# Kernel tuning notes

Measured on AMD Instinct MI355X. Metric: run time of the kernel, lower is better.

Reference implementation:

```python
import jax, jax.numpy as jnp
import numpy as np

B, N, DIM = 2, 2048, 1024
HEADS, DIM_HEAD, ROT = 16, 64, 32
SCALE = DIM_HEAD ** -0.5
INNER = HEADS * DIM_HEAD


def rotate_half(x):
    # '... (j d) -> ... j d' with j=2 -> split into first/second half
    d = x.shape[-1] // 2
    x1, x2 = x[..., :d], x[..., d:]
    return jnp.concatenate([-x2, x1], axis=-1)


def apply_rotary_pos_emb(freqs, t):
    rot = freqs.shape[-1]
    t1, t_pass = t[..., :rot], t[..., rot:]
    t1 = t1 * jnp.cos(freqs) + rotate_half(t1) * jnp.sin(freqs)
    return jnp.concatenate([t1, t_pass], axis=-1)


def setup_inputs() -> dict:
    key = jax.random.key(0)
    ks = jax.random.split(key, 5)
    x = jax.random.normal(ks[0], (B, N, DIM), dtype=jnp.float32)
    mask = jnp.ones((B, N), dtype=bool)
    rotary_pos_emb = jax.random.normal(ks[1], (N, ROT), dtype=jnp.float32)
    w_qkv = jax.random.normal(ks[2], (DIM, 3 * INNER), dtype=jnp.float32) * (DIM ** -0.5)
    w_out = jax.random.normal(ks[3], (INNER, DIM), dtype=jnp.float32) * (INNER ** -0.5)
    g = jnp.ones((DIM,), dtype=jnp.float32)
    return {"x": x, "mask": mask, "rotary_pos_emb": rotary_pos_emb,
            "w_qkv": w_qkv, "w_out": w_out, "g": g}


def reference(x, mask, rotary_pos_emb, w_qkv, w_out, g):
    b, n, _ = x.shape
    qkv = x @ w_qkv  # [b, n, 3*inner]
    q, k, v = jnp.split(qkv, 3, axis=-1)
    def to_heads(t):
        return t.reshape(b, n, HEADS, DIM_HEAD).transpose(0, 2, 1, 3)  # b h n d
    q, k, v = to_heads(q), to_heads(k), to_heads(v)
    q = q * SCALE
    # note: original applies rotary to q, k AND v
    q = apply_rotary_pos_emb(rotary_pos_emb, q)
    k = apply_rotary_pos_emb(rotary_pos_emb, k)
    v = apply_rotary_pos_emb(rotary_pos_emb, v)
    sim = jnp.einsum('bhid,bhjd->bhij', q, k)  # [b, h, n, n]
    neg = -jnp.finfo(sim.dtype).max
    sim = jnp.where(mask[:, None, None, :], sim, neg)
    causal_mask = jnp.triu(jnp.ones((n, n), dtype=bool), 1)
    sim = jnp.where(causal_mask, neg, sim)
    attn = jax.nn.softmax(sim.astype(jnp.float32), axis=-1).astype(sim.dtype)
    out = jnp.einsum('bhij,bhjd->bhid', attn, v)
    out = out.transpose(0, 2, 1, 3).reshape(b, n, INNER)
    out = out @ w_out
    # LayerNorm (no bias), eps=1e-5 for fp32, biased variance
    mean = jnp.mean(out, axis=-1, keepdims=True)
    var = jnp.var(out, axis=-1, keepdims=True)
    return (out - mean) * jax.lax.rsqrt(var + 1e-5) * g
```

## Files before the change

kernel.cpp:

```cpp
#include <hip/hip_runtime.h>
#include <stdint.h>

typedef unsigned short u16;
typedef __bf16 bf16x8 __attribute__((ext_vector_type(8)));
typedef float f32x4 __attribute__((ext_vector_type(4)));

#define B_ 2
#define N_ 2048
#define H_ 16
#define SCALE_ 0.125f
#define FM_ 11.0f

__device__ __forceinline__ float b2f(u16 u) {
    unsigned v = (unsigned)u << 16;
    float f;
    __builtin_memcpy(&f, &v, 4);
    return f;
}
__device__ __forceinline__ u16 f2b(float f) {
    unsigned x;
    __builtin_memcpy(&x, &f, 4);
    x = x + 0x7fff + ((x >> 16) & 1);
    return (u16)(x >> 16);
}
__device__ __forceinline__ unsigned fbits(float f) {
    unsigned x;
    __builtin_memcpy(&x, &f, 4);
    return x;
}

typedef const __attribute__((address_space(1))) unsigned int ga_uint;
typedef __attribute__((address_space(3))) unsigned int ls_uint;
__device__ __forceinline__ void gld_lds16(const void* g, void* l) {
    __builtin_amdgcn_global_load_lds((ga_uint*)g, (ls_uint*)l, 16, 0, 0);
}

#define MFMA_ __builtin_amdgcn_mfma_f32_16x16x32_bf16
#define ZERO4_ ((f32x4){0.f, 0.f, 0.f, 0.f})

__global__ __launch_bounds__(256) void sentinel(float* __restrict__ out, int n, float val) {
    int i = blockIdx.x * 256 + threadIdx.x;
    if (i < n) out[i] = val;
}

__global__ __launch_bounds__(256) void prep(const float* __restrict__ rotf,
                                            float* __restrict__ ct, float* __restrict__ st,
                                            const float* __restrict__ x, u16* __restrict__ xbf,
                                            const float* __restrict__ wqkv, u16* __restrict__ wqkvT,
                                            const float* __restrict__ wout, u16* __restrict__ woutT) {
    __shared__ float tile[32][33];
    int bid = blockIdx.x;
    const int tid = threadIdx.x;
    if (bid < 256) {
        int i = bid * 256 + tid;
        float f = rotf[i];
        ct[i] = cosf(f);
        st[i] = sinf(f);
        return;
    }
    bid -= 256;
    if (bid < 4096) {
        int i = (bid * 256 + tid) * 4;
        float4 v = *(const float4*)(x + i);
        ushort4 o;
        o.x = f2b(v.x); o.y = f2b(v.y); o.z = f2b(v.z); o.w = f2b(v.w);
        *(ushort4*)(xbf + i) = o;
        return;
    }
    bid -= 4096;
    const float* in;
    u16* out;
    int C, bx, by;
    if (bid < 3072) {
        in = wqkv; out = wqkvT; C = 3072; bx = bid % 96; by = bid / 96;
    } else {
        bid -= 3072;
        in = wout; out = woutT; C = 1024; bx = bid % 32; by = bid / 32;
    }
    const int R = 1024;
    int tx = tid & 31, ty = tid >> 5;
    int c0 = bx * 32, r0 = by * 32;
#pragma unroll
    for (int i = 0; i < 32; i += 8) tile[ty + i][tx] = in[(size_t)(r0 + ty + i) * C + c0 + tx];
    __syncthreads();
#pragma unroll
    for (int i = 0; i < 32; i += 8) out[(size_t)(c0 + ty + i) * R + r0 + tx] = f2b(tile[tx][ty + i]);
}

__global__ __launch_bounds__(256) void gemm_qkv(const u16* __restrict__ A, const u16* __restrict__ Bt,
                                                const float* __restrict__ ct, const float* __restrict__ st,
                                                u16* __restrict__ qo, u16* __restrict__ ko,
                                                u16* __restrict__ vt) {
    __shared__ __align__(16) u16 As[128 * 32];
    __shared__ __align__(16) u16 Bs[128 * 32];
    const int tid = threadIdx.x;
    const int wave = tid >> 6, lane = tid & 63;
    const int l15 = lane & 15, q4 = lane >> 4;
    const int id = blockIdx.x;
    const int xcd = id & 7, slot = id >> 3;
    const int nt = (xcd & 1) * 12 + (slot % 12);
    const int mt = (xcd >> 1) * 8 + (slot / 12);
    const int m0 = mt * 128, n0 = nt * 128;
    const int wm = (wave & 1) * 64, wn = (wave >> 1) * 64;
    const int lrow = lane >> 2, lchunk = (lane & 3) * 8;
    f32x4 c00 = ZERO4_, c01 = ZERO4_, c02 = ZERO4_, c03 = ZERO4_;
    f32x4 c10 = ZERO4_, c11 = ZERO4_, c12 = ZERO4_, c13 = ZERO4_;
    f32x4 c20 = ZERO4_, c21 = ZERO4_, c22 = ZERO4_, c23 = ZERO4_;
    f32x4 c30 = ZERO4_, c31 = ZERO4_, c32 = ZERO4_, c33 = ZERO4_;

    for (int k0 = 0; k0 < 1024; k0 += 32) {
        {
            int r0_ = wave * 32, r1_ = r0_ + 16;
            gld_lds16(&A[(size_t)(m0 + r0_ + lrow) * 1024 + k0 + lchunk], &As[r0_ * 32]);
            gld_lds16(&Bt[(size_t)(n0 + r0_ + lrow) * 1024 + k0 + lchunk], &Bs[r0_ * 32]);
            gld_lds16(&A[(size_t)(m0 + r1_ + lrow) * 1024 + k0 + lchunk], &As[r1_ * 32]);
            gld_lds16(&Bt[(size_t)(n0 + r1_ + lrow) * 1024 + k0 + lchunk], &Bs[r1_ * 32]);
        }
        __syncthreads();
        bf16x8 a0 = *(const bf16x8*)&As[(wm + l15) * 32 + q4 * 8];
        bf16x8 a1 = *(const bf16x8*)&As[(wm + 16 + l15) * 32 + q4 * 8];
        bf16x8 a2 = *(const bf16x8*)&As[(wm + 32 + l15) * 32 + q4 * 8];
        bf16x8 a3 = *(const bf16x8*)&As[(wm + 48 + l15) * 32 + q4 * 8];
        bf16x8 b0 = *(const bf16x8*)&Bs[(wn + l15) * 32 + q4 * 8];
        bf16x8 b1 = *(const bf16x8*)&Bs[(wn + 16 + l15) * 32 + q4 * 8];
        bf16x8 b2 = *(const bf16x8*)&Bs[(wn + 32 + l15) * 32 + q4 * 8];
        bf16x8 b3 = *(const bf16x8*)&Bs[(wn + 48 + l15) * 32 + q4 * 8];
        c00 = MFMA_(a0, b0, c00, 0, 0, 0); c01 = MFMA_(a0, b1, c01, 0, 0, 0);
        c02 = MFMA_(a0, b2, c02, 0, 0, 0); c03 = MFMA_(a0, b3, c03, 0, 0, 0);
        c10 = MFMA_(a1, b0, c10, 0, 0, 0); c11 = MFMA_(a1, b1, c11, 0, 0, 0);
        c12 = MFMA_(a1, b2, c12, 0, 0, 0); c13 = MFMA_(a1, b3, c13, 0, 0, 0);
        c20 = MFMA_(a2, b0, c20, 0, 0, 0); c21 = MFMA_(a2, b1, c21, 0, 0, 0);
        c22 = MFMA_(a2, b2, c22, 0, 0, 0); c23 = MFMA_(a2, b3, c23, 0, 0, 0);
        c30 = MFMA_(a3, b0, c30, 0, 0, 0); c31 = MFMA_(a3, b1, c31, 0, 0, 0);
        c32 = MFMA_(a3, b2, c32, 0, 0, 0); c33 = MFMA_(a3, b3, c33, 0, 0, 0);
        __syncthreads();
    }
    const int qh = n0 + wn;
    const int t = qh >> 10;
    const int h = (qh & 1023) >> 6;
    auto epi = [&](int mtb, f32x4 x0v, f32x4 x1v, f32x4 x2v, f32x4 x3v) {
#pragma unroll
        for (int r = 0; r < 4; r++) {
            int gm = m0 + wm + mtb + q4 * 4 + r;
            int b = gm >> 11, n = gm & 2047;
            float x0 = x0v[r], x1 = x1v[r], x2 = x2v[r], x3 = x3v[r];
            float c1 = ct[n * 32 + l15], s1 = st[n * 32 + l15];
            float c2 = ct[n * 32 + 16 + l15], s2 = st[n * 32 + 16 + l15];
            if (t == 0) { x0 *= SCALE_; x1 *= SCALE_; x2 *= SCALE_; x3 *= SCALE_; }
            float r0 = x0 * c1 - x1 * s1;
            float r1 = x1 * c2 + x0 * s2;
            int bh = b * H_ + h;
            if (t == 2) {
                u16* o = vt + (size_t)bh * 64 * N_;
                o[(l15) * N_ + n] = f2b(r0);
                o[(l15 + 16) * N_ + n] = f2b(r1);
                o[(l15 + 32) * N_ + n] = f2b(x2);
                o[(l15 + 48) * N_ + n] = f2b(x3);
            } else {
                u16* dst = (t == 0) ? qo : ko;
                u16* p = dst + ((size_t)bh * N_ + n) * 64;
                p[l15] = f2b(r0);
                p[l15 + 16] = f2b(r1);
                p[l15 + 32] = f2b(x2);
                p[l15 + 48] = f2b(x3);
            }
        }
    };
    epi(0, c00, c01, c02, c03);
    epi(16, c10, c11, c12, c13);
    epi(32, c20, c21, c22, c23);
    epi(48, c30, c31, c32, c33);
}

__global__ __launch_bounds__(256) void attn(const u16* __restrict__ q, const u16* __restrict__ k,
                                            const u16* __restrict__ vt, u16* __restrict__ out) {
    __shared__ __align__(16) u16 Ks[2][64 * 72];
    __shared__ __align__(16) u16 Vs[2][64 * 72];
    __shared__ __align__(16) u16 Ps[64 * 72];
    const int tid = threadIdx.x, wave = tid >> 6, lane = tid & 63;
    const int l15 = lane & 15, q4 = lane >> 4;
    const int id = blockIdx.x;
    const int slot = id >> 3;
    const int bh = (id & 7) * 4 + (slot >> 4);
    const int ta = slot & 15, tb = 31 - ta;
    const u16* qp = q + (size_t)bh * N_ * 64;
    const u16* kp = k + (size_t)bh * N_ * 64;
    const u16* vp = vt + (size_t)bh * 64 * N_;
    const int b = bh >> 4, h = bh & 15;
    const int srow8 = tid >> 3, scol8 = (tid & 7) * 8;
    const int prow = (wave * 16 + l15) * 72;

    bf16x8 aqA0, aqA1, aqB0, aqB1;
    {
        int qr = ta * 64 + wave * 16;
        aqA0 = *(const bf16x8*)&qp[(qr + l15) * 64 + q4 * 8];
        aqA1 = *(const bf16x8*)&qp[(qr + l15) * 64 + 32 + q4 * 8];
        qr = tb * 64 + wave * 16;
        aqB0 = *(const bf16x8*)&qp[(qr + l15) * 64 + q4 * 8];
        aqB1 = *(const bf16x8*)&qp[(qr + l15) * 64 + 32 + q4 * 8];
    }
    f32x4 o[4];
#pragma unroll
    for (int i = 0; i < 4; i++) o[i] = ZERO4_;
    float psum = 0.f;

    auto stage = [&](int jt, int buf) {
#pragma unroll
        for (int i = 0; i < 64; i += 32) {
            *(uint4*)&Ks[buf][(i + srow8) * 72 + scol8] =
                *(const uint4*)&kp[(size_t)(jt * 64 + i + srow8) * 64 + scol8];
            *(uint4*)&Vs[buf][(i + srow8) * 72 + scol8] =
                *(const uint4*)&vp[(size_t)(i + srow8) * N_ + jt * 64 + scol8];
        }
    };
    auto iter = [&](bf16x8 aq0, bf16x8 aq1, int cur, int domask, int qa, int jb) {
#pragma unroll
        for (int kt = 0; kt < 4; kt++) {
            bf16x8 kf0 = *(const bf16x8*)&Ks[cur][(kt * 16 + l15) * 72 + q4 * 8];
            bf16x8 kf1 = *(const bf16x8*)&Ks[cur][(kt * 16 + l15) * 72 + 32 + q4 * 8];
            f32x4 z = ZERO4_;
            z = MFMA_(kf0, aq0, z, 0, 0, 0);
            z = MFMA_(kf1, aq1, z, 0, 0, 0);
            float p0, p1, p2, p3;
            {
                float s0 = z[0], s1 = z[1], s2 = z[2], s3 = z[3];
                if (domask) {
                    int key = jb * 64 + kt * 16 + q4 * 4;
                    if (key + 0 > qa) s0 = -1e30f;
                    if (key + 1 > qa) s1 = -1e30f;
                    if (key + 2 > qa) s2 = -1e30f;
                    if (key + 3 > qa) s3 = -1e30f;
                }
                p0 = __expf(s0 - FM_); p1 = __expf(s1 - FM_);
                p2 = __expf(s2 - FM_); p3 = __expf(s3 - FM_);
            }
            psum += (p0 + p1) + (p2 + p3);
            uint2 pk;
            pk.x = __builtin_amdgcn_perm(fbits(p1), fbits(p0), 0x07060302u);
            pk.y = __builtin_amdgcn_perm(fbits(p3), fbits(p2), 0x07060302u);
            *(uint2*)&Ps[prow + kt * 16 + q4 * 4] = pk;
        }
        bf16x8 pf0 = *(const bf16x8*)&Ps[prow + q4 * 8];
        bf16x8 pf1 = *(const bf16x8*)&Ps[prow + 32 + q4 * 8];
#pragma unroll
        for (int dt = 0; dt < 4; dt++) {
            bf16x8 v0 = *(const bf16x8*)&Vs[cur][(dt * 16 + l15) * 72 + q4 * 8];
            bf16x8 v1 = *(const bf16x8*)&Vs[cur][(dt * 16 + l15) * 72 + 32 + q4 * 8];
            o[dt] = MFMA_(v0, pf0, o[dt], 0, 0, 0);
            o[dt] = MFMA_(v1, pf1, o[dt], 0, 0, 0);
        }
    };
    auto epilogue = [&](int qt) {
        float v = psum;
        v += __shfl_xor(v, 16);
        v += __shfl_xor(v, 32);
        float inv = 1.f / v;
        int n = qt * 64 + wave * 16 + l15;
        u16* op = out + ((size_t)b * N_ + n) * 1024 + h * 64;
#pragma unroll
        for (int dt = 0; dt < 4; dt++) {
            union { u16 u[4]; uint2 v2; } w;
#pragma unroll
            for (int r = 0; r < 4; r++) w.u[r] = f2b(o[dt][r] * inv);
            *(uint2*)(op + dt * 16 + q4 * 4) = w.v2;
        }
#pragma unroll
        for (int i = 0; i < 4; i++) o[i] = ZERO4_;
        psum = 0.f;
    };

    stage(0, 0);
    int m = 0;
    for (int jb = 0; jb <= ta; jb++, m++) {
        int cur = m & 1;
        __syncthreads();
        stage((jb < ta) ? (jb + 1) : 0, cur ^ 1);
        iter(aqA0, aqA1, cur, jb == ta, ta * 64 + wave * 16 + l15, jb);
    }
    epilogue(ta);
    for (int jb = 0; jb <= tb; jb++, m++) {
        int cur = m & 1;
        __syncthreads();
        if (jb < tb) stage(jb + 1, cur ^ 1);
        iter(aqB0, aqB1, cur, jb == tb, tb * 64 + wave * 16 + l15, jb);
    }
    epilogue(tb);
}

__global__ __launch_bounds__(256) void gemm_out(const u16* __restrict__ A, const u16* __restrict__ Bt,
                                                float* __restrict__ C) {
    __shared__ __align__(16) u16 As[128 * 32];
    __shared__ __align__(16) u16 Bs[128 * 32];
    const int tid = threadIdx.x;
    const int wave = tid >> 6, lane = tid & 63;
    const int l15 = lane & 15, q4 = lane >> 4;
    const int id = blockIdx.x;
    const int xcd = id & 7, slot = id >> 3;
    const int mt = xcd * 4 + (slot >> 3);
    const int nt = slot & 7;
    const int m0 = mt * 128, n0 = nt * 128;
    const int wm = (wave & 1) * 64, wn = (wave >> 1) * 64;
    const int lrow = lane >> 2, lchunk = (lane & 3) * 8;
    f32x4 c00 = ZERO4_, c01 = ZERO4_, c02 = ZERO4_, c03 = ZERO4_;
    f32x4 c10 = ZERO4_, c11 = ZERO4_, c12 = ZERO4_, c13 = ZERO4_;
    f32x4 c20 = ZERO4_, c21 = ZERO4_, c22 = ZERO4_, c23 = ZERO4_;
    f32x4 c30 = ZERO4_, c31 = ZERO4_, c32 = ZERO4_, c33 = ZERO4_;

    for (int k0 = 0; k0 < 1024; k0 += 32) {
        {
            int r0_ = wave * 32, r1_ = r0_ + 16;
            gld_lds16(&A[(size_t)(m0 + r0_ + lrow) * 1024 + k0 + lchunk], &As[r0_ * 32]);
            gld_lds16(&Bt[(size_t)(n0 + r0_ + lrow) * 1024 + k0 + lchunk], &Bs[r0_ * 32]);
            gld_lds16(&A[(size_t)(m0 + r1_ + lrow) * 1024 + k0 + lchunk], &As[r1_ * 32]);
            gld_lds16(&Bt[(size_t)(n0 + r1_ + lrow) * 1024 + k0 + lchunk], &Bs[r1_ * 32]);
        }
        __syncthreads();
        bf16x8 a0 = *(const bf16x8*)&As[(wm + l15) * 32 + q4 * 8];
        bf16x8 a1 = *(const bf16x8*)&As[(wm + 16 + l15) * 32 + q4 * 8];
        bf16x8 a2 = *(const bf16x8*)&As[(wm + 32 + l15) * 32 + q4 * 8];
        bf16x8 a3 = *(const bf16x8*)&As[(wm + 48 + l15) * 32 + q4 * 8];
        bf16x8 b0 = *(const bf16x8*)&Bs[(wn + l15) * 32 + q4 * 8];
        bf16x8 b1 = *(const bf16x8*)&Bs[(wn + 16 + l15) * 32 + q4 * 8];
        bf16x8 b2 = *(const bf16x8*)&Bs[(wn + 32 + l15) * 32 + q4 * 8];
        bf16x8 b3 = *(const bf16x8*)&Bs[(wn + 48 + l15) * 32 + q4 * 8];
        c00 = MFMA_(a0, b0, c00, 0, 0, 0); c01 = MFMA_(a0, b1, c01, 0, 0, 0);
        c02 = MFMA_(a0, b2, c02, 0, 0, 0); c03 = MFMA_(a0, b3, c03, 0, 0, 0);
        c10 = MFMA_(a1, b0, c10, 0, 0, 0); c11 = MFMA_(a1, b1, c11, 0, 0, 0);
        c12 = MFMA_(a1, b2, c12, 0, 0, 0); c13 = MFMA_(a1, b3, c13, 0, 0, 0);
        c20 = MFMA_(a2, b0, c20, 0, 0, 0); c21 = MFMA_(a2, b1, c21, 0, 0, 0);
        c22 = MFMA_(a2, b2, c22, 0, 0, 0); c23 = MFMA_(a2, b3, c23, 0, 0, 0);
        c30 = MFMA_(a3, b0, c30, 0, 0, 0); c31 = MFMA_(a3, b1, c31, 0, 0, 0);
        c32 = MFMA_(a3, b2, c32, 0, 0, 0); c33 = MFMA_(a3, b3, c33, 0, 0, 0);
        __syncthreads();
    }
    auto sto = [&](int mtb, int ntb, f32x4 c) {
#pragma unroll
        for (int r = 0; r < 4; r++) {
            int gm = m0 + wm + mtb + q4 * 4 + r;
            int gn = n0 + wn + ntb + l15;
            C[(size_t)gm * 1024 + gn] = c[r];
        }
    };
    sto(0, 0, c00);  sto(0, 16, c01);  sto(0, 32, c02);  sto(0, 48, c03);
    sto(16, 0, c10); sto(16, 16, c11); sto(16, 32, c12); sto(16, 48, c13);
    sto(32, 0, c20); sto(32, 16, c21); sto(32, 32, c22); sto(32, 48, c23);
    sto(48, 0, c30); sto(48, 16, c31); sto(48, 32, c32); sto(48, 48, c33);
}

__global__ __launch_bounds__(256) void lnorm(const float* __restrict__ x, const float* __restrict__ g,
                                             float* __restrict__ out) {
    __shared__ float sh[8];
    int row = blockIdx.x, tid = threadIdx.x;
    float4 v = *(const float4*)(x + (size_t)row * 1024 + tid * 4);
    float s = v.x + v.y + v.z + v.w;
    float sq = v.x * v.x + v.y * v.y + v.z * v.z + v.w * v.w;
#pragma unroll
    for (int m = 1; m < 64; m <<= 1) {
        s += __shfl_xor(s, m);
        sq += __shfl_xor(sq, m);
    }
    if ((tid & 63) == 0) {
        sh[tid >> 6] = s;
        sh[4 + (tid >> 6)] = sq;
    }
    __syncthreads();
    s = sh[0] + sh[1] + sh[2] + sh[3];
    sq = sh[4] + sh[5] + sh[6] + sh[7];
    float mean = s * (1.f / 1024.f);
    float var = fmaxf(sq * (1.f / 1024.f) - mean * mean, 0.f);
    float rstd = rsqrtf(var + 1e-5f);
    float4 gv = *(const float4*)(g + tid * 4);
    float4 ov;
    ov.x = (v.x - mean) * rstd * gv.x;
    ov.y = (v.y - mean) * rstd * gv.y;
    ov.z = (v.z - mean) * rstd * gv.z;
    ov.w = (v.w - mean) * rstd * gv.w;
    *(float4*)(out + (size_t)row * 1024 + tid * 4) = ov;
}

extern "C" void kernel_launch(void* const* d_in, const int* in_sizes, int n_in,
                              void* d_out, int out_size, void* d_ws, size_t ws_size,
                              hipStream_t stream) {
    const float* x = nullptr;
    const float* rotf = nullptr;
    const float* wqkv = nullptr;
    const float* wout = nullptr;
    const float* g = nullptr;
    for (int i = 0; i < n_in; i++) {
        switch (in_sizes[i]) {
            case 4194304: x = (const float*)d_in[i]; break;
            case 65536:   rotf = (const float*)d_in[i]; break;
            case 3145728: wqkv = (const float*)d_in[i]; break;
            case 1048576: wout = (const float*)d_in[i]; break;
            case 1024:    g = (const float*)d_in[i]; break;
            default: break;
        }
    }
    int oblk = (out_size + 255) / 256;
    if (!(x && rotf && wqkv && wout && g)) {
        sentinel<<<oblk, 256, 0, stream>>>((float*)d_out, out_size, 200.f);
        return;
    }
    const size_t MB = 1024u * 1024;
    if (ws_size < 80 * MB) {
        sentinel<<<oblk, 256, 0, stream>>>((float*)d_out, out_size, 100.f);
        return;
    }
    char* ws = (char*)d_ws;
    u16* wqkvT = (u16*)(ws);
    u16* woutT = (u16*)(ws + 6 * MB);
    u16* xbf = (u16*)(ws + 8 * MB);
    u16* qbuf = (u16*)(ws + 16 * MB);
    u16* kbuf = (u16*)(ws + 24 * MB);
    u16* vtbuf = (u16*)(ws + 32 * MB);
    u16* abuf = (u16*)(ws + 40 * MB);
    float* pbuf = (float*)(ws + 48 * MB);
    float* ctab = (float*)(ws + 64 * MB);
    float* stab = (float*)(ws + 64 * MB + 256 * 1024);

    prep<<<8448, 256, 0, stream>>>(rotf, ctab, stab, x, xbf, wqkv, wqkvT, wout, woutT);
    gemm_qkv<<<768, 256, 0, stream>>>(xbf, wqkvT, ctab, stab, qbuf, kbuf, vtbuf);
    attn<<<512, 256, 0, stream>>>(qbuf, kbuf, vtbuf, abuf);
    gemm_out<<<256, 256, 0, stream>>>(abuf, woutT, pbuf);
    lnorm<<<4096, 256, 0, stream>>>(pbuf, g, (float*)d_out);
}
```

Before: 203.5 us.

## Double-buffer and swizzle LDS tiles in QKV and output GEMMs

Both projection GEMMs switch from a single LDS tile with two syncthreads per k-step to a two-stage double buffer. The next tile's global-to-LDS loads are issued before the MFMAs, with explicit vmcnt/lgkmcnt waits, raw s_barrier and sched_barrier fences. The LDS layout is XOR-swizzled by row, with the inverse mapping applied to the global source addresses, to cut bank conflicts on the 16-byte fragment reads. s_setprio raises wave priority around the MFMA block; the cost is double the LDS footprint and more hand-ordered synchronization.

```diff
diff --git a/kernel.cpp b/kernel.cpp
--- a/kernel.cpp
+++ b/kernel.cpp
@@ -87,12 +87,21 @@
     for (int i = 0; i < 32; i += 8) out[(size_t)(c0 + ty + i) * R + r0 + tx] = f2b(tile[tx][ty + i]);
 }
 
+__device__ __forceinline__ int swz_off(int row, int c16) {
+    return (((row * 64 + c16 * 16) ^ ((row & 7) << 4)) >> 1);
+}
+__device__ __forceinline__ void swz_inv(int W, int& r, int& c16) {
+    int rh = W >> 7;
+    r = (rh << 1) | (((W >> 6) & 1) ^ ((rh >> 1) & 1));
+    c16 = ((W >> 4) & 3) ^ (r & 3);
+}
+
 __global__ __launch_bounds__(256) void gemm_qkv(const u16* __restrict__ A, const u16* __restrict__ Bt,
                                                 const float* __restrict__ ct, const float* __restrict__ st,
                                                 u16* __restrict__ qo, u16* __restrict__ ko,
                                                 u16* __restrict__ vt) {
-    __shared__ __align__(16) u16 As[128 * 32];
-    __shared__ __align__(16) u16 Bs[128 * 32];
+    __shared__ __align__(16) u16 As[2][128 * 32];
+    __shared__ __align__(16) u16 Bs[2][128 * 32];
     const int tid = threadIdx.x;
     const int wave = tid >> 6, lane = tid & 63;
     const int l15 = lane & 15, q4 = lane >> 4;
@@ -102,29 +111,55 @@
     const int mt = (xcd >> 1) * 8 + (slot / 12);
     const int m0 = mt * 128, n0 = nt * 128;
     const int wm = (wave & 1) * 64, wn = (wave >> 1) * 64;
-    const int lrow = lane >> 2, lchunk = (lane & 3) * 8;
+
+    int rS0, cS0, rS1, cS1;
+    swz_inv((wave * 32) * 64 + lane * 16, rS0, cS0);
+    swz_inv((wave * 32 + 16) * 64 + lane * 16, rS1, cS1);
+    const u16* aS0 = A + (size_t)(m0 + rS0) * 1024 + cS0 * 8;
+    const u16* aS1 = A + (size_t)(m0 + rS1) * 1024 + cS1 * 8;
+    const u16* bS0 = Bt + (size_t)(n0 + rS0) * 1024 + cS0 * 8;
+    const u16* bS1 = Bt + (size_t)(n0 + rS1) * 1024 + cS1 * 8;
+
+    auto stage = [&](int buf, int k0) {
+        gld_lds16(aS0 + k0, &As[buf][(wave * 32) * 32]);
+        gld_lds16(bS0 + k0, &Bs[buf][(wave * 32) * 32]);
+        gld_lds16(aS1 + k0, &As[buf][(wave * 32 + 16) * 32]);
+        gld_lds16(bS1 + k0, &Bs[buf][(wave * 32 + 16) * 32]);
+    };
+    const int oa0 = swz_off(wm + l15, q4), oa1 = swz_off(wm + 16 + l15, q4),
+              oa2 = swz_off(wm + 32 + l15, q4), oa3 = swz_off(wm + 48 + l15, q4);
+    const int ob0 = swz_off(wn + l15, q4), ob1 = swz_off(wn + 16 + l15, q4),
+              ob2 = swz_off(wn + 32 + l15, q4), ob3 = swz_off(wn + 48 + l15, q4);
+
     f32x4 c00 = ZERO4_, c01 = ZERO4_, c02 = ZERO4_, c03 = ZERO4_;
     f32x4 c10 = ZERO4_, c11 = ZERO4_, c12 = ZERO4_, c13 = ZERO4_;
     f32x4 c20 = ZERO4_, c21 = ZERO4_, c22 = ZERO4_, c23 = ZERO4_;
     f32x4 c30 = ZERO4_, c31 = ZERO4_, c32 = ZERO4_, c33 = ZERO4_;
 
-    for (int k0 = 0; k0 < 1024; k0 += 32) {
-        {
-            int r0_ = wave * 32, r1_ = r0_ + 16;
-            gld_lds16(&A[(size_t)(m0 + r0_ + lrow) * 1024 + k0 + lchunk], &As[r0_ * 32]);
-            gld_lds16(&Bt[(size_t)(n0 + r0_ + lrow) * 1024 + k0 + lchunk], &Bs[r0_ * 32]);
-            gld_lds16(&A[(size_t)(m0 + r1_ + lrow) * 1024 + k0 + lchunk], &As[r1_ * 32]);
-            gld_lds16(&Bt[(size_t)(n0 + r1_ + lrow) * 1024 + k0 + lchunk], &Bs[r1_ * 32]);
-        }
-        __syncthreads();
-        bf16x8 a0 = *(const bf16x8*)&As[(wm + l15) * 32 + q4 * 8];
-        bf16x8 a1 = *(const bf16x8*)&As[(wm + 16 + l15) * 32 + q4 * 8];
-        bf16x8 a2 = *(const bf16x8*)&As[(wm + 32 + l15) * 32 + q4 * 8];
-        bf16x8 a3 = *(const bf16x8*)&As[(wm + 48 + l15) * 32 + q4 * 8];
-        bf16x8 b0 = *(const bf16x8*)&Bs[(wn + l15) * 32 + q4 * 8];
-        bf16x8 b1 = *(const bf16x8*)&Bs[(wn + 16 + l15) * 32 + q4 * 8];
-        bf16x8 b2 = *(const bf16x8*)&Bs[(wn + 32 + l15) * 32 + q4 * 8];
-        bf16x8 b3 = *(const bf16x8*)&Bs[(wn + 48 + l15) * 32 + q4 * 8];
+    stage(0, 0);
+    stage(1, 32);
+    int kNext = 64;
+    for (int i = 0; i < 31; ++i) {
+        const int cur = i & 1;
+        asm volatile("s_waitcnt vmcnt(4)" ::: "memory");
+        __builtin_amdgcn_sched_barrier(0);
+        __builtin_amdgcn_s_barrier();
+        __builtin_amdgcn_sched_barrier(0);
+        bf16x8 a0 = *(const bf16x8*)&As[cur][oa0];
+        bf16x8 a1 = *(const bf16x8*)&As[cur][oa1];
+        bf16x8 a2 = *(const bf16x8*)&As[cur][oa2];
+        bf16x8 a3 = *(const bf16x8*)&As[cur][oa3];
+        bf16x8 b0 = *(const bf16x8*)&Bs[cur][ob0];
+        bf16x8 b1 = *(const bf16x8*)&Bs[cur][ob1];
+        bf16x8 b2 = *(const bf16x8*)&Bs[cur][ob2];
+        bf16x8 b3 = *(const bf16x8*)&Bs[cur][ob3];
+        asm volatile("s_waitcnt lgkmcnt(0)" ::: "memory");
+        __builtin_amdgcn_sched_barrier(0);
+        __builtin_amdgcn_s_barrier();
+        __builtin_amdgcn_sched_barrier(0);
+        if (i < 30) { stage(cur, kNext); kNext += 32; }
+        __builtin_amdgcn_sched_barrier(0);
+        __builtin_amdgcn_s_setprio(1);
         c00 = MFMA_(a0, b0, c00, 0, 0, 0); c01 = MFMA_(a0, b1, c01, 0, 0, 0);
         c02 = MFMA_(a0, b2, c02, 0, 0, 0); c03 = MFMA_(a0, b3, c03, 0, 0, 0);
         c10 = MFMA_(a1, b0, c10, 0, 0, 0); c11 = MFMA_(a1, b1, c11, 0, 0, 0);
@@ -133,7 +168,29 @@
         c22 = MFMA_(a2, b2, c22, 0, 0, 0); c23 = MFMA_(a2, b3, c23, 0, 0, 0);
         c30 = MFMA_(a3, b0, c30, 0, 0, 0); c31 = MFMA_(a3, b1, c31, 0, 0, 0);
         c32 = MFMA_(a3, b2, c32, 0, 0, 0); c33 = MFMA_(a3, b3, c33, 0, 0, 0);
-        __syncthreads();
+        __builtin_amdgcn_s_setprio(0);
+    }
+    {
+        asm volatile("s_waitcnt vmcnt(0)" ::: "memory");
+        __builtin_amdgcn_sched_barrier(0);
+        __builtin_amdgcn_s_barrier();
+        __builtin_amdgcn_sched_barrier(0);
+        bf16x8 a0 = *(const bf16x8*)&As[1][oa0];
+        bf16x8 a1 = *(const bf16x8*)&As[1][oa1];
+        bf16x8 a2 = *(const bf16x8*)&As[1][oa2];
+        bf16x8 a3 = *(const bf16x8*)&As[1][oa3];
+        bf16x8 b0 = *(const bf16x8*)&Bs[1][ob0];
+        bf16x8 b1 = *(const bf16x8*)&Bs[1][ob1];
+        bf16x8 b2 = *(const bf16x8*)&Bs[1][ob2];
+        bf16x8 b3 = *(const bf16x8*)&Bs[1][ob3];
+        c00 = MFMA_(a0, b0, c00, 0, 0, 0); c01 = MFMA_(a0, b1, c01, 0, 0, 0);
+        c02 = MFMA_(a0, b2, c02, 0, 0, 0); c03 = MFMA_(a0, b3, c03, 0, 0, 0);
+        c10 = MFMA_(a1, b0, c10, 0, 0, 0); c11 = MFMA_(a1, b1, c11, 0, 0, 0);
+        c12 = MFMA_(a1, b2, c12, 0, 0, 0); c13 = MFMA_(a1, b3, c13, 0, 0, 0);
+        c20 = MFMA_(a2, b0, c20, 0, 0, 0); c21 = MFMA_(a2, b1, c21, 0, 0, 0);
+        c22 = MFMA_(a2, b2, c22, 0, 0, 0); c23 = MFMA_(a2, b3, c23, 0, 0, 0);
+        c30 = MFMA_(a3, b0, c30, 0, 0, 0); c31 = MFMA_(a3, b1, c31, 0, 0, 0);
+        c32 = MFMA_(a3, b2, c32, 0, 0, 0); c33 = MFMA_(a3, b3, c33, 0, 0, 0);
     }
     const int qh = n0 + wn;
     const int t = qh >> 10;
@@ -289,8 +346,8 @@
 
 __global__ __launch_bounds__(256) void gemm_out(const u16* __restrict__ A, const u16* __restrict__ Bt,
                                                 float* __restrict__ C) {
-    __shared__ __align__(16) u16 As[128 * 32];
-    __shared__ __align__(16) u16 Bs[128 * 32];
+    __shared__ __align__(16) u16 As[2][128 * 32];
+    __shared__ __align__(16) u16 Bs[2][128 * 32];
     const int tid = threadIdx.x;
     const int wave = tid >> 6, lane = tid & 63;
     const int l15 = lane & 15, q4 = lane >> 4;
@@ -300,29 +357,55 @@
     const int nt = slot & 7;
     const int m0 = mt * 128, n0 = nt * 128;
     const int wm = (wave & 1) * 64, wn = (wave >> 1) * 64;
-    const int lrow = lane >> 2, lchunk = (lane & 3) * 8;
+
+    int rS0, cS0, rS1, cS1;
+    swz_inv((wave * 32) * 64 + lane * 16, rS0, cS0);
+    swz_inv((wave * 32 + 16) * 64 + lane * 16, rS1, cS1);
+    const u16* aS0 = A + (size_t)(m0 + rS0) * 1024 + cS0 * 8;
+    const u16* aS1 = A + (size_t)(m0 + rS1) * 1024 + cS1 * 8;
+    const u16* bS0 = Bt + (size_t)(n0 + rS0) * 1024 + cS0 * 8;
+    const u16* bS1 = Bt + (size_t)(n0 + rS1) * 1024 + cS1 * 8;
+
+    auto stage = [&](int buf, int k0) {
+        gld_lds16(aS0 + k0, &As[buf][(wave * 32) * 32]);
+        gld_lds16(bS0 + k0, &Bs[buf][(wave * 32) * 32]);
+        gld_lds16(aS1 + k0, &As[buf][(wave * 32 + 16) * 32]);
+        gld_lds16(bS1 + k0, &Bs[buf][(wave * 32 + 16) * 32]);
+    };
+    const int oa0 = swz_off(wm + l15, q4), oa1 = swz_off(wm + 16 + l15, q4),
+              oa2 = swz_off(wm + 32 + l15, q4), oa3 = swz_off(wm + 48 + l15, q4);
+    const int ob0 = swz_off(wn + l15, q4), ob1 = swz_off(wn + 16 + l15, q4),
+              ob2 = swz_off(wn + 32 + l15, q4), ob3 = swz_off(wn + 48 + l15, q4);
+
     f32x4 c00 = ZERO4_, c01 = ZERO4_, c02 = ZERO4_, c03 = ZERO4_;
     f32x4 c10 = ZERO4_, c11 = ZERO4_, c12 = ZERO4_, c13 = ZERO4_;
     f32x4 c20 = ZERO4_, c21 = ZERO4_, c22 = ZERO4_, c23 = ZERO4_;
     f32x4 c30 = ZERO4_, c31 = ZERO4_, c32 = ZERO4_, c33 = ZERO4_;
 
-    for (int k0 = 0; k0 < 1024; k0 += 32) {
-        {
-            int r0_ = wave * 32, r1_ = r0_ + 16;
-            gld_lds16(&A[(size_t)(m0 + r0_ + lrow) * 1024 + k0 + lchunk], &As[r0_ * 32]);
-            gld_lds16(&Bt[(size_t)(n0 + r0_ + lrow) * 1024 + k0 + lchunk], &Bs[r0_ * 32]);
-            gld_lds16(&A[(size_t)(m0 + r1_ + lrow) * 1024 + k0 + lchunk], &As[r1_ * 32]);
-            gld_lds16(&Bt[(size_t)(n0 + r1_ + lrow) * 1024 + k0 + lchunk], &Bs[r1_ * 32]);
-        }
-        __syncthreads();
-        bf16x8 a0 = *(const bf16x8*)&As[(wm + l15) * 32 + q4 * 8];
-        bf16x8 a1 = *(const bf16x8*)&As[(wm + 16 + l15) * 32 + q4 * 8];
-        bf16x8 a2 = *(const bf16x8*)&As[(wm + 32 + l15) * 32 + q4 * 8];
-        bf16x8 a3 = *(const bf16x8*)&As[(wm + 48 + l15) * 32 + q4 * 8];
-        bf16x8 b0 = *(const bf16x8*)&Bs[(wn + l15) * 32 + q4 * 8];
-        bf16x8 b1 = *(const bf16x8*)&Bs[(wn + 16 + l15) * 32 + q4 * 8];
-        bf16x8 b2 = *(const bf16x8*)&Bs[(wn + 32 + l15) * 32 + q4 * 8];
-        bf16x8 b3 = *(const bf16x8*)&Bs[(wn + 48 + l15) * 32 + q4 * 8];
+    stage(0, 0);
+    stage(1, 32);
+    int kNext = 64;
+    for (int i = 0; i < 31; ++i) {
+        const int cur = i & 1;
+        asm volatile("s_waitcnt vmcnt(4)" ::: "memory");
+        __builtin_amdgcn_sched_barrier(0);
+        __builtin_amdgcn_s_barrier();
+        __builtin_amdgcn_sched_barrier(0);
+        bf16x8 a0 = *(const bf16x8*)&As[cur][oa0];
+        bf16x8 a1 = *(const bf16x8*)&As[cur][oa1];
+        bf16x8 a2 = *(const bf16x8*)&As[cur][oa2];
+        bf16x8 a3 = *(const bf16x8*)&As[cur][oa3];
+        bf16x8 b0 = *(const bf16x8*)&Bs[cur][ob0];
+        bf16x8 b1 = *(const bf16x8*)&Bs[cur][ob1];
+        bf16x8 b2 = *(const bf16x8*)&Bs[cur][ob2];
+        bf16x8 b3 = *(const bf16x8*)&Bs[cur][ob3];
+        asm volatile("s_waitcnt lgkmcnt(0)" ::: "memory");
+        __builtin_amdgcn_sched_barrier(0);
+        __builtin_amdgcn_s_barrier();
+        __builtin_amdgcn_sched_barrier(0);
+        if (i < 30) { stage(cur, kNext); kNext += 32; }
+        __builtin_amdgcn_sched_barrier(0);
+        __builtin_amdgcn_s_setprio(1);
         c00 = MFMA_(a0, b0, c00, 0, 0, 0); c01 = MFMA_(a0, b1, c01, 0, 0, 0);
         c02 = MFMA_(a0, b2, c02, 0, 0, 0); c03 = MFMA_(a0, b3, c03, 0, 0, 0);
         c10 = MFMA_(a1, b0, c10, 0, 0, 0); c11 = MFMA_(a1, b1, c11, 0, 0, 0);
@@ -331,7 +414,29 @@
         c22 = MFMA_(a2, b2, c22, 0, 0, 0); c23 = MFMA_(a2, b3, c23, 0, 0, 0);
         c30 = MFMA_(a3, b0, c30, 0, 0, 0); c31 = MFMA_(a3, b1, c31, 0, 0, 0);
         c32 = MFMA_(a3, b2, c32, 0, 0, 0); c33 = MFMA_(a3, b3, c33, 0, 0, 0);
-        __syncthreads();
+        __builtin_amdgcn_s_setprio(0);
+    }
+    {
+        asm volatile("s_waitcnt vmcnt(0)" ::: "memory");
+        __builtin_amdgcn_sched_barrier(0);
+        __builtin_amdgcn_s_barrier();
+        __builtin_amdgcn_sched_barrier(0);
+        bf16x8 a0 = *(const bf16x8*)&As[1][oa0];
+        bf16x8 a1 = *(const bf16x8*)&As[1][oa1];
+        bf16x8 a2 = *(const bf16x8*)&As[1][oa2];
+        bf16x8 a3 = *(const bf16x8*)&As[1][oa3];
+        bf16x8 b0 = *(const bf16x8*)&Bs[1][ob0];
+        bf16x8 b1 = *(const bf16x8*)&Bs[1][ob1];
+        bf16x8 b2 = *(const bf16x8*)&Bs[1][ob2];
+        bf16x8 b3 = *(const bf16x8*)&Bs[1][ob3];
+        c00 = MFMA_(a0, b0, c00, 0, 0, 0); c01 = MFMA_(a0, b1, c01, 0, 0, 0);
+        c02 = MFMA_(a0, b2, c02, 0, 0, 0); c03 = MFMA_(a0, b3, c03, 0, 0, 0);
+        c10 = MFMA_(a1, b0, c10, 0, 0, 0); c11 = MFMA_(a1, b1, c11, 0, 0, 0);
+        c12 = MFMA_(a1, b2, c12, 0, 0, 0); c13 = MFMA_(a1, b3, c13, 0, 0, 0);
+        c20 = MFMA_(a2, b0, c20, 0, 0, 0); c21 = MFMA_(a2, b1, c21, 0, 0, 0);
+        c22 = MFMA_(a2, b2, c22, 0, 0, 0); c23 = MFMA_(a2, b3, c23, 0, 0, 0);
+        c30 = MFMA_(a3, b0, c30, 0, 0, 0); c31 = MFMA_(a3, b1, c31, 0, 0, 0);
+        c32 = MFMA_(a3, b2, c32, 0, 0, 0); c33 = MFMA_(a3, b3, c33, 0, 0, 0);
     }
     auto sto = [&](int mtb, int ntb, f32x4 c) {
 #pragma unroll
```

Measured after the change: 217.0 us. 6.7% more time.

## Double-buffer LDS in both GEMMs and prefetch K/V tiles into registers in attention

Applied to the files above, without the earlier changes.

Both projection GEMMs now use two LDS buffers, issuing the next k-slice's global-to-LDS loads before computing on the current one, which removes one barrier per iteration. The attention kernel splits staging into a register prefetch issued one tile ahead and an LDS write after compute, using a single barrier with an explicit lgkmcnt wait. This is meant to hide global load latency behind MFMA work. The cost is doubled LDS use in the GEMMs, extra VGPRs in attention, and subtle ordering hazards: the GEMM loop relies on async LDS loads completing before the barrier (no explicit vmcnt wait shown), and reads of the current buffer may race with writes to the other buffer across iterations.

```diff
diff --git a/kernel.cpp b/kernel.cpp
--- a/kernel.cpp
+++ b/kernel.cpp
@@ -91,8 +91,8 @@
                                                 const float* __restrict__ ct, const float* __restrict__ st,
                                                 u16* __restrict__ qo, u16* __restrict__ ko,
                                                 u16* __restrict__ vt) {
-    __shared__ __align__(16) u16 As[128 * 32];
-    __shared__ __align__(16) u16 Bs[128 * 32];
+    __shared__ __align__(16) u16 As[2][128 * 32];
+    __shared__ __align__(16) u16 Bs[2][128 * 32];
     const int tid = threadIdx.x;
     const int wave = tid >> 6, lane = tid & 63;
     const int l15 = lane & 15, q4 = lane >> 4;
@@ -103,28 +103,33 @@
     const int m0 = mt * 128, n0 = nt * 128;
     const int wm = (wave & 1) * 64, wn = (wave >> 1) * 64;
     const int lrow = lane >> 2, lchunk = (lane & 3) * 8;
+
+    auto stage = [&](int buf, int k0) {
+        int r0_ = wave * 32, r1_ = r0_ + 16;
+        gld_lds16(&A[(size_t)(m0 + r0_ + lrow) * 1024 + k0 + lchunk], &As[buf][r0_ * 32]);
+        gld_lds16(&Bt[(size_t)(n0 + r0_ + lrow) * 1024 + k0 + lchunk], &Bs[buf][r0_ * 32]);
+        gld_lds16(&A[(size_t)(m0 + r1_ + lrow) * 1024 + k0 + lchunk], &As[buf][r1_ * 32]);
+        gld_lds16(&Bt[(size_t)(n0 + r1_ + lrow) * 1024 + k0 + lchunk], &Bs[buf][r1_ * 32]);
+    };
+
     f32x4 c00 = ZERO4_, c01 = ZERO4_, c02 = ZERO4_, c03 = ZERO4_;
     f32x4 c10 = ZERO4_, c11 = ZERO4_, c12 = ZERO4_, c13 = ZERO4_;
     f32x4 c20 = ZERO4_, c21 = ZERO4_, c22 = ZERO4_, c23 = ZERO4_;
     f32x4 c30 = ZERO4_, c31 = ZERO4_, c32 = ZERO4_, c33 = ZERO4_;
 
-    for (int k0 = 0; k0 < 1024; k0 += 32) {
-        {
-            int r0_ = wave * 32, r1_ = r0_ + 16;
-            gld_lds16(&A[(size_t)(m0 + r0_ + lrow) * 1024 + k0 + lchunk], &As[r0_ * 32]);
-            gld_lds16(&Bt[(size_t)(n0 + r0_ + lrow) * 1024 + k0 + lchunk], &Bs[r0_ * 32]);
-            gld_lds16(&A[(size_t)(m0 + r1_ + lrow) * 1024 + k0 + lchunk], &As[r1_ * 32]);
-            gld_lds16(&Bt[(size_t)(n0 + r1_ + lrow) * 1024 + k0 + lchunk], &Bs[r1_ * 32]);
-        }
-        __syncthreads();
-        bf16x8 a0 = *(const bf16x8*)&As[(wm + l15) * 32 + q4 * 8];
-        bf16x8 a1 = *(const bf16x8*)&As[(wm + 16 + l15) * 32 + q4 * 8];
-        bf16x8 a2 = *(const bf16x8*)&As[(wm + 32 + l15) * 32 + q4 * 8];
-        bf16x8 a3 = *(const bf16x8*)&As[(wm + 48 + l15) * 32 + q4 * 8];
-        bf16x8 b0 = *(const bf16x8*)&Bs[(wn + l15) * 32 + q4 * 8];
-        bf16x8 b1 = *(const bf16x8*)&Bs[(wn + 16 + l15) * 32 + q4 * 8];
-        bf16x8 b2 = *(const bf16x8*)&Bs[(wn + 32 + l15) * 32 + q4 * 8];
-        bf16x8 b3 = *(const bf16x8*)&Bs[(wn + 48 + l15) * 32 + q4 * 8];
+    stage(0, 0);
+    __syncthreads();
+    for (int t = 0; t < 32; ++t) {
+        const int cur = t & 1;
+        if (t < 31) stage(cur ^ 1, (t + 1) * 32);
+        bf16x8 a0 = *(const bf16x8*)&As[cur][(wm + l15) * 32 + q4 * 8];
+        bf16x8 a1 = *(const bf16x8*)&As[cur][(wm + 16 + l15) * 32 + q4 * 8];
+        bf16x8 a2 = *(const bf16x8*)&As[cur][(wm + 32 + l15) * 32 + q4 * 8];
+        bf16x8 a3 = *(const bf16x8*)&As[cur][(wm + 48 + l15) * 32 + q4 * 8];
+        bf16x8 b0 = *(const bf16x8*)&Bs[cur][(wn + l15) * 32 + q4 * 8];
+        bf16x8 b1 = *(const bf16x8*)&Bs[cur][(wn + 16 + l15) * 32 + q4 * 8];
+        bf16x8 b2 = *(const bf16x8*)&Bs[cur][(wn + 32 + l15) * 32 + q4 * 8];
+        bf16x8 b3 = *(const bf16x8*)&Bs[cur][(wn + 48 + l15) * 32 + q4 * 8];
         c00 = MFMA_(a0, b0, c00, 0, 0, 0); c01 = MFMA_(a0, b1, c01, 0, 0, 0);
         c02 = MFMA_(a0, b2, c02, 0, 0, 0); c03 = MFMA_(a0, b3, c03, 0, 0, 0);
         c10 = MFMA_(a1, b0, c10, 0, 0, 0); c11 = MFMA_(a1, b1, c11, 0, 0, 0);
@@ -133,7 +138,7 @@
         c22 = MFMA_(a2, b2, c22, 0, 0, 0); c23 = MFMA_(a2, b3, c23, 0, 0, 0);
         c30 = MFMA_(a3, b0, c30, 0, 0, 0); c31 = MFMA_(a3, b1, c31, 0, 0, 0);
         c32 = MFMA_(a3, b2, c32, 0, 0, 0); c33 = MFMA_(a3, b3, c33, 0, 0, 0);
-        __syncthreads();
+        if (t < 31) __syncthreads();
     }
     const int qh = n0 + wn;
     const int t = qh >> 10;
@@ -204,15 +209,21 @@
     for (int i = 0; i < 4; i++) o[i] = ZERO4_;
     float psum = 0.f;
 
-    auto stage = [&](int jt, int buf) {
-#pragma unroll
-        for (int i = 0; i < 64; i += 32) {
-            *(uint4*)&Ks[buf][(i + srow8) * 72 + scol8] =
-                *(const uint4*)&kp[(size_t)(jt * 64 + i + srow8) * 64 + scol8];
-            *(uint4*)&Vs[buf][(i + srow8) * 72 + scol8] =
-                *(const uint4*)&vp[(size_t)(i + srow8) * N_ + jt * 64 + scol8];
-        }
-    };
+    uint4 LK0, LK1, LV0, LV1;
+    auto ldissue = [&](int jt) {
+        LK0 = *(const uint4*)&kp[(size_t)(jt * 64 + srow8) * 64 + scol8];
+        LK1 = *(const uint4*)&kp[(size_t)(jt * 64 + 32 + srow8) * 64 + scol8];
+        LV0 = *(const uint4*)&vp[(size_t)srow8 * N_ + jt * 64 + scol8];
+        LV1 = *(const uint4*)&vp[(size_t)(32 + srow8) * N_ + jt * 64 + scol8];
+    };
+    auto wrbuf = [&](int buf) {
+        *(uint4*)&Ks[buf][srow8 * 72 + scol8] = LK0;
+        *(uint4*)&Ks[buf][(32 + srow8) * 72 + scol8] = LK1;
+        *(uint4*)&Vs[buf][srow8 * 72 + scol8] = LV0;
+        *(uint4*)&Vs[buf][(32 + srow8) * 72 + scol8] = LV1;
+    };
+    auto tileof = [&](int i) { return (i <= ta) ? i : i - ta - 1; };
+
     auto iter = [&](bf16x8 aq0, bf16x8 aq1, int cur, int domask, int qa, int jb) {
 #pragma unroll
         for (int kt = 0; kt < 4; kt++) {
@@ -269,28 +280,36 @@
         psum = 0.f;
     };
 
-    stage(0, 0);
+    ldissue(0);
+    wrbuf(0);
+    ldissue(tileof(1));
     int m = 0;
     for (int jb = 0; jb <= ta; jb++, m++) {
-        int cur = m & 1;
-        __syncthreads();
-        stage((jb < ta) ? (jb + 1) : 0, cur ^ 1);
+        const int cur = m & 1;
+        asm volatile("s_waitcnt lgkmcnt(0)" ::: "memory");
+        __builtin_amdgcn_s_barrier();
         iter(aqA0, aqA1, cur, jb == ta, ta * 64 + wave * 16 + l15, jb);
+        wrbuf(cur ^ 1);
+        ldissue(tileof(m + 2));
     }
     epilogue(ta);
     for (int jb = 0; jb <= tb; jb++, m++) {
-        int cur = m & 1;
-        __syncthreads();
-        if (jb < tb) stage(jb + 1, cur ^ 1);
+        const int cur = m & 1;
+        asm volatile("s_waitcnt lgkmcnt(0)" ::: "memory");
+        __builtin_amdgcn_s_barrier();
         iter(aqB0, aqB1, cur, jb == tb, tb * 64 + wave * 16 + l15, jb);
+        if (m < 32) {
+            wrbuf(cur ^ 1);
+            if (m < 31) ldissue(tileof(m + 2));
+        }
     }
     epilogue(tb);
 }
 
 __global__ __launch_bounds__(256) void gemm_out(const u16* __restrict__ A, const u16* __restrict__ Bt,
                                                 float* __restrict__ C) {
-    __shared__ __align__(16) u16 As[128 * 32];
-    __shared__ __align__(16) u16 Bs[128 * 32];
+    __shared__ __align__(16) u16 As[2][128 * 32];
+    __shared__ __align__(16) u16 Bs[2][128 * 32];
     const int tid = threadIdx.x;
     const int wave = tid >> 6, lane = tid & 63;
     const int l15 = lane & 15, q4 = lane >> 4;
@@ -301,28 +320,33 @@
     const int m0 = mt * 128, n0 = nt * 128;
     const int wm = (wave & 1) * 64, wn = (wave >> 1) * 64;
     const int lrow = lane >> 2, lchunk = (lane & 3) * 8;
+
+    auto stage = [&](int buf, int k0) {
+        int r0_ = wave * 32, r1_ = r0_ + 16;
+        gld_lds16(&A[(size_t)(m0 + r0_ + lrow) * 1024 + k0 + lchunk], &As[buf][r0_ * 32]);
+        gld_lds16(&Bt[(size_t)(n0 + r0_ + lrow) * 1024 + k0 + lchunk], &Bs[buf][r0_ * 32]);
+        gld_lds16(&A[(size_t)(m0 + r1_ + lrow) * 1024 + k0 + lchunk], &As[buf][r1_ * 32]);
+        gld_lds16(&Bt[(size_t)(n0 + r1_ + lrow) * 1024 + k0 + lchunk], &Bs[buf][r1_ * 32]);
+    };
+
     f32x4 c00 = ZERO4_, c01 = ZERO4_, c02 = ZERO4_, c03 = ZERO4_;
     f32x4 c10 = ZERO4_, c11 = ZERO4_, c12 = ZERO4_, c13 = ZERO4_;
     f32x4 c20 = ZERO4_, c21 = ZERO4_, c22 = ZERO4_, c23 = ZERO4_;
     f32x4 c30 = ZERO4_, c31 = ZERO4_, c32 = ZERO4_, c33 = ZERO4_;
 
-    for (int k0 = 0; k0 < 1024; k0 += 32) {
-        {
-            int r0_ = wave * 32, r1_ = r0_ + 16;
-            gld_lds16(&A[(size_t)(m0 + r0_ + lrow) * 1024 + k0 + lchunk], &As[r0_ * 32]);
-            gld_lds16(&Bt[(size_t)(n0 + r0_ + lrow) * 1024 + k0 + lchunk], &Bs[r0_ * 32]);
-            gld_lds16(&A[(size_t)(m0 + r1_ + lrow) * 1024 + k0 + lchunk], &As[r1_ * 32]);
-            gld_lds16(&Bt[(size_t)(n0 + r1_ + lrow) * 1024 + k0 + lchunk], &Bs[r1_ * 32]);
-        }
-        __syncthreads();
-        bf16x8 a0 = *(const bf16x8*)&As[(wm + l15) * 32 + q4 * 8];
-        bf16x8 a1 = *(const bf16x8*)&As[(wm + 16 + l15) * 32 + q4 * 8];
-        bf16x8 a2 = *(const bf16x8*)&As[(wm + 32 + l15) * 32 + q4 * 8];
-        bf16x8 a3 = *(const bf16x8*)&As[(wm + 48 + l15) * 32 + q4 * 8];
-        bf16x8 b0 = *(const bf16x8*)&Bs[(wn + l15) * 32 + q4 * 8];
-        bf16x8 b1 = *(const bf16x8*)&Bs[(wn + 16 + l15) * 32 + q4 * 8];
-        bf16x8 b2 = *(const bf16x8*)&Bs[(wn + 32 + l15) * 32 + q4 * 8];
-        bf16x8 b3 = *(const bf16x8*)&Bs[(wn + 48 + l15) * 32 + q4 * 8];
+    stage(0, 0);
+    __syncthreads();
+    for (int t = 0; t < 32; ++t) {
+        const int cur = t & 1;
+        if (t < 31) stage(cur ^ 1, (t + 1) * 32);
+        bf16x8 a0 = *(const bf16x8*)&As[cur][(wm + l15) * 32 + q4 * 8];
+        bf16x8 a1 = *(const bf16x8*)&As[cur][(wm + 16 + l15) * 32 + q4 * 8];
+        bf16x8 a2 = *(const bf16x8*)&As[cur][(wm + 32 + l15) * 32 + q4 * 8];
+        bf16x8 a3 = *(const bf16x8*)&As[cur][(wm + 48 + l15) * 32 + q4 * 8];
+        bf16x8 b0 = *(const bf16x8*)&Bs[cur][(wn + l15) * 32 + q4 * 8];
+        bf16x8 b1 = *(const bf16x8*)&Bs[cur][(wn + 16 + l15) * 32 + q4 * 8];
+        bf16x8 b2 = *(const bf16x8*)&Bs[cur][(wn + 32 + l15) * 32 + q4 * 8];
+        bf16x8 b3 = *(const bf16x8*)&Bs[cur][(wn + 48 + l15) * 32 + q4 * 8];
         c00 = MFMA_(a0, b0, c00, 0, 0, 0); c01 = MFMA_(a0, b1, c01, 0, 0, 0);
         c02 = MFMA_(a0, b2, c02, 0, 0, 0); c03 = MFMA_(a0, b3, c03, 0, 0, 0);
         c10 = MFMA_(a1, b0, c10, 0, 0, 0); c11 = MFMA_(a1, b1, c11, 0, 0, 0);
@@ -331,7 +355,7 @@
         c22 = MFMA_(a2, b2, c22, 0, 0, 0); c23 = MFMA_(a2, b3, c23, 0, 0, 0);
         c30 = MFMA_(a3, b0, c30, 0, 0, 0); c31 = MFMA_(a3, b1, c31, 0, 0, 0);
         c32 = MFMA_(a3, b2, c32, 0, 0, 0); c33 = MFMA_(a3, b3, c33, 0, 0, 0);
-        __syncthreads();
+        if (t < 31) __syncthreads();
     }
     auto sto = [&](int mtb, int ntb, f32x4 c) {
 #pragma unroll
```

After: 201.3 us. Within noise of the previous version (-1.1%).

## Register-prefetch K/V tiles in attention and halve gemm_out N-tile

Applied to the files above, without the earlier changes.

The attention loop now loads the next K/V tile from global memory into registers one iteration ahead and writes it into the other LDS buffer after the MFMA work. It uses a raw s_barrier with an lgkmcnt wait in place of __syncthreads, so global load latency overlaps compute instead of stalling before each barrier. Separately, gemm_out drops from 128x128 to 128x64 tiles and launches 512 blocks instead of 256, to fill more CUs on the 1024-wide output. The cost is more register pressure in attention and less reuse of A per block in the GEMM.

```diff
diff --git a/kernel.cpp b/kernel.cpp
--- a/kernel.cpp
+++ b/kernel.cpp
@@ -204,15 +204,21 @@
     for (int i = 0; i < 4; i++) o[i] = ZERO4_;
     float psum = 0.f;
 
-    auto stage = [&](int jt, int buf) {
-#pragma unroll
-        for (int i = 0; i < 64; i += 32) {
-            *(uint4*)&Ks[buf][(i + srow8) * 72 + scol8] =
-                *(const uint4*)&kp[(size_t)(jt * 64 + i + srow8) * 64 + scol8];
-            *(uint4*)&Vs[buf][(i + srow8) * 72 + scol8] =
-                *(const uint4*)&vp[(size_t)(i + srow8) * N_ + jt * 64 + scol8];
-        }
-    };
+    uint4 LK0, LK1, LV0, LV1;
+    auto ldissue = [&](int jt) {
+        LK0 = *(const uint4*)&kp[(size_t)(jt * 64 + srow8) * 64 + scol8];
+        LK1 = *(const uint4*)&kp[(size_t)(jt * 64 + 32 + srow8) * 64 + scol8];
+        LV0 = *(const uint4*)&vp[(size_t)srow8 * N_ + jt * 64 + scol8];
+        LV1 = *(const uint4*)&vp[(size_t)(32 + srow8) * N_ + jt * 64 + scol8];
+    };
+    auto wrbuf = [&](int buf) {
+        *(uint4*)&Ks[buf][srow8 * 72 + scol8] = LK0;
+        *(uint4*)&Ks[buf][(32 + srow8) * 72 + scol8] = LK1;
+        *(uint4*)&Vs[buf][srow8 * 72 + scol8] = LV0;
+        *(uint4*)&Vs[buf][(32 + srow8) * 72 + scol8] = LV1;
+    };
+    auto tileof = [&](int i) { return (i <= ta) ? i : i - ta - 1; };
+
     auto iter = [&](bf16x8 aq0, bf16x8 aq1, int cur, int domask, int qa, int jb) {
 #pragma unroll
         for (int kt = 0; kt < 4; kt++) {
@@ -269,20 +275,28 @@
         psum = 0.f;
     };
 
-    stage(0, 0);
+    ldissue(0);
+    wrbuf(0);
+    ldissue(tileof(1));
     int m = 0;
     for (int jb = 0; jb <= ta; jb++, m++) {
-        int cur = m & 1;
-        __syncthreads();
-        stage((jb < ta) ? (jb + 1) : 0, cur ^ 1);
+        const int cur = m & 1;
+        asm volatile("s_waitcnt lgkmcnt(0)" ::: "memory");
+        __builtin_amdgcn_s_barrier();
         iter(aqA0, aqA1, cur, jb == ta, ta * 64 + wave * 16 + l15, jb);
+        wrbuf(cur ^ 1);
+        ldissue(tileof(m + 2));
     }
     epilogue(ta);
     for (int jb = 0; jb <= tb; jb++, m++) {
-        int cur = m & 1;
-        __syncthreads();
-        if (jb < tb) stage(jb + 1, cur ^ 1);
+        const int cur = m & 1;
+        asm volatile("s_waitcnt lgkmcnt(0)" ::: "memory");
+        __builtin_amdgcn_s_barrier();
         iter(aqB0, aqB1, cur, jb == tb, tb * 64 + wave * 16 + l15, jb);
+        if (m < 32) {
+            wrbuf(cur ^ 1);
+            if (m < 31) ldissue(tileof(m + 2));
+        }
     }
     epilogue(tb);
 }
@@ -290,29 +304,29 @@
 __global__ __launch_bounds__(256) void gemm_out(const u16* __restrict__ A, const u16* __restrict__ Bt,
                                                 float* __restrict__ C) {
     __shared__ __align__(16) u16 As[128 * 32];
-    __shared__ __align__(16) u16 Bs[128 * 32];
+    __shared__ __align__(16) u16 Bs[64 * 32];
     const int tid = threadIdx.x;
     const int wave = tid >> 6, lane = tid & 63;
     const int l15 = lane & 15, q4 = lane >> 4;
     const int id = blockIdx.x;
     const int xcd = id & 7, slot = id >> 3;
-    const int mt = xcd * 4 + (slot >> 3);
-    const int nt = slot & 7;
-    const int m0 = mt * 128, n0 = nt * 128;
-    const int wm = (wave & 1) * 64, wn = (wave >> 1) * 64;
+    const int mt = xcd * 4 + (slot >> 4);
+    const int nt = slot & 15;
+    const int m0 = mt * 128, n0 = nt * 64;
+    const int wm = (wave & 1) * 64, wn = (wave >> 1) * 32;
     const int lrow = lane >> 2, lchunk = (lane & 3) * 8;
-    f32x4 c00 = ZERO4_, c01 = ZERO4_, c02 = ZERO4_, c03 = ZERO4_;
-    f32x4 c10 = ZERO4_, c11 = ZERO4_, c12 = ZERO4_, c13 = ZERO4_;
-    f32x4 c20 = ZERO4_, c21 = ZERO4_, c22 = ZERO4_, c23 = ZERO4_;
-    f32x4 c30 = ZERO4_, c31 = ZERO4_, c32 = ZERO4_, c33 = ZERO4_;
+
+    f32x4 c00 = ZERO4_, c01 = ZERO4_;
+    f32x4 c10 = ZERO4_, c11 = ZERO4_;
+    f32x4 c20 = ZERO4_, c21 = ZERO4_;
+    f32x4 c30 = ZERO4_, c31 = ZERO4_;
 
     for (int k0 = 0; k0 < 1024; k0 += 32) {
         {
             int r0_ = wave * 32, r1_ = r0_ + 16;
             gld_lds16(&A[(size_t)(m0 + r0_ + lrow) * 1024 + k0 + lchunk], &As[r0_ * 32]);
-            gld_lds16(&Bt[(size_t)(n0 + r0_ + lrow) * 1024 + k0 + lchunk], &Bs[r0_ * 32]);
             gld_lds16(&A[(size_t)(m0 + r1_ + lrow) * 1024 + k0 + lchunk], &As[r1_ * 32]);
-            gld_lds16(&Bt[(size_t)(n0 + r1_ + lrow) * 1024 + k0 + lchunk], &Bs[r1_ * 32]);
+            gld_lds16(&Bt[(size_t)(n0 + wave * 16 + lrow) * 1024 + k0 + lchunk], &Bs[(wave * 16) * 32]);
         }
         __syncthreads();
         bf16x8 a0 = *(const bf16x8*)&As[(wm + l15) * 32 + q4 * 8];
@@ -321,16 +335,10 @@
         bf16x8 a3 = *(const bf16x8*)&As[(wm + 48 + l15) * 32 + q4 * 8];
         bf16x8 b0 = *(const bf16x8*)&Bs[(wn + l15) * 32 + q4 * 8];
         bf16x8 b1 = *(const bf16x8*)&Bs[(wn + 16 + l15) * 32 + q4 * 8];
-        bf16x8 b2 = *(const bf16x8*)&Bs[(wn + 32 + l15) * 32 + q4 * 8];
-        bf16x8 b3 = *(const bf16x8*)&Bs[(wn + 48 + l15) * 32 + q4 * 8];
         c00 = MFMA_(a0, b0, c00, 0, 0, 0); c01 = MFMA_(a0, b1, c01, 0, 0, 0);
-        c02 = MFMA_(a0, b2, c02, 0, 0, 0); c03 = MFMA_(a0, b3, c03, 0, 0, 0);
         c10 = MFMA_(a1, b0, c10, 0, 0, 0); c11 = MFMA_(a1, b1, c11, 0, 0, 0);
-        c12 = MFMA_(a1, b2, c12, 0, 0, 0); c13 = MFMA_(a1, b3, c13, 0, 0, 0);
         c20 = MFMA_(a2, b0, c20, 0, 0, 0); c21 = MFMA_(a2, b1, c21, 0, 0, 0);
-        c22 = MFMA_(a2, b2, c22, 0, 0, 0); c23 = MFMA_(a2, b3, c23, 0, 0, 0);
         c30 = MFMA_(a3, b0, c30, 0, 0, 0); c31 = MFMA_(a3, b1, c31, 0, 0, 0);
-        c32 = MFMA_(a3, b2, c32, 0, 0, 0); c33 = MFMA_(a3, b3, c33, 0, 0, 0);
         __syncthreads();
     }
     auto sto = [&](int mtb, int ntb, f32x4 c) {
@@ -341,10 +349,10 @@
             C[(size_t)gm * 1024 + gn] = c[r];
         }
     };
-    sto(0, 0, c00);  sto(0, 16, c01);  sto(0, 32, c02);  sto(0, 48, c03);
-    sto(16, 0, c10); sto(16, 16, c11); sto(16, 32, c12); sto(16, 48, c13);
-    sto(32, 0, c20); sto(32, 16, c21); sto(32, 32, c22); sto(32, 48, c23);
-    sto(48, 0, c30); sto(48, 16, c31); sto(48, 32, c32); sto(48, 48, c33);
+    sto(0, 0, c00);  sto(0, 16, c01);
+    sto(16, 0, c10); sto(16, 16, c11);
+    sto(32, 0, c20); sto(32, 16, c21);
+    sto(48, 0, c30); sto(48, 16, c31);
 }
 
 __global__ __launch_bounds__(256) void lnorm(const float* __restrict__ x, const float* __restrict__ g,
@@ -421,6 +429,6 @@
     prep<<<8448, 256, 0, stream>>>(rotf, ctab, stab, x, xbf, wqkv, wqkvT, wout, woutT);
     gemm_qkv<<<768, 256, 0, stream>>>(xbf, wqkvT, ctab, stab, qbuf, kbuf, vtbuf);
     attn<<<512, 256, 0, stream>>>(qbuf, kbuf, vtbuf, abuf);
-    gemm_out<<<256, 256, 0, stream>>>(abuf, woutT, pbuf);
+    gemm_out<<<512, 256, 0, stream>>>(abuf, woutT, pbuf);
     lnorm<<<4096, 256, 0, stream>>>(pbuf, g, (float*)d_out);
 }
```

New measurement: 197.4 us (median of 3 runs). 1.03x faster.
